# Optimization experiments

Measured on AMD Instinct MI355X. Metric: run time of the kernel, lower is better.

Reference implementation:

```python
import jax, jax.numpy as jnp
import numpy as np

N = 50000      # nodes
E = 800000     # edges
DIN = 500      # input feature dim
H = 128        # hidden dim
C = 40         # num classes
B = 10000      # batch_size (labeled nodes)
L = 9          # n_layers
K = 5          # topk neighbors
ALPHA = 0.5
THETA = 1.0
ETA = 0.5


def setup_inputs() -> dict:
    key = jax.random.key(0)
    ks = jax.random.split(key, 10)
    x = jax.random.normal(ks[0], (N, DIN), jnp.float32)
    edge_index = jax.random.randint(ks[1], (2, E), 0, N, dtype=jnp.int32)
    edge_weight = jax.random.uniform(ks[2], (E,), jnp.float32)
    y = jax.random.randint(ks[3], (B,), 0, C, dtype=jnp.int32)
    W1 = jax.random.normal(ks[4], (DIN, H), jnp.float32) * 0.05
    b1 = jnp.zeros((H,), jnp.float32)
    conv_w1 = jax.random.normal(ks[5], (L, H, H), jnp.float32) * 0.05
    conv_w2 = jax.random.normal(ks[6], (L, H, H), jnp.float32) * 0.05
    W2 = jax.random.normal(ks[7], (H, C), jnp.float32) * 0.05
    b2 = jnp.zeros((C,), jnp.float32)
    return dict(x=x, edge_index=edge_index, edge_weight=edge_weight, y=y,
                batch_size=B, W1=W1, b1=b1, conv_w1=conv_w1, conv_w2=conv_w2,
                W2=W2, b2=b2)


def _spmm(edge_index, edge_weight, h):
    # out[row] += w * h[col]  (sparse adj_t @ h)
    row, col = edge_index[0], edge_index[1]
    msg = h[col] * edge_weight[:, None]           # [E, H]
    return jax.ops.segment_sum(msg, row, num_segments=N)


def reference(x, edge_index, edge_weight, y, batch_size, W1, b1, conv_w1, conv_w2, W2, b2):
    # eval mode: dropout is identity, no diagonal mask in label fusion
    h = jax.nn.relu(x @ W1 + b1)                  # [N, H]
    x0 = h
    for l in range(L):
        beta = float(np.log(THETA / (l + 1) + 1.0))
        p = _spmm(edge_index, edge_weight, h) * (1.0 - ALPHA)   # propagated, scaled
        xr = ALPHA * x0                                          # initial residual
        out = ((1.0 - beta) * p + beta * (p @ conv_w1[l])
               + (1.0 - beta) * xr + beta * (xr @ conv_w2[l]))
        h = jax.nn.relu(h + out)
    emb = h[:batch_size]                          # [B, H]
    logits = h @ W2 + b2
    p_lc = jax.nn.log_softmax(logits[:batch_size], axis=1)       # [B, C]
    # kNN label fusion: cosine similarity, topk, exp-weighted one-hot sum
    an = emb / jnp.clip(jnp.linalg.norm(emb, axis=1, keepdims=True), 1e-8)
    sim = an @ an.T                               # [B, B]
    vals, idx = jax.lax.top_k(sim, K)             # [B, K]
    w = jnp.exp(jax.lax.stop_gradient(vals))      # topk computed under no_grad
    onehot = jax.nn.one_hot(y, C, dtype=jnp.float32)             # [B, C]
    fused = jnp.einsum('bk,bkc->bc', w, onehot[idx])             # [B, C]
    p_sim = jax.nn.log_softmax(fused, axis=1)
    final = ETA * p_lc + (1.0 - ETA) * p_sim
    return final, emb
```

## Files before the change

### kernel.cpp

```cpp
#include <hip/hip_runtime.h>
#include <hip/hip_bf16.h>
#include <math.h>

#define Nn  50000
#define NR  50048
#define En  800000
#define DIN 500
#define Hd  128
#define Cc  40
#define Bb  10000
#define Ll  9
#define KT  5

typedef short bf16x8 __attribute__((ext_vector_type(8)));
typedef unsigned short u16x8 __attribute__((ext_vector_type(8)));
typedef float f32x4 __attribute__((ext_vector_type(4)));

__device__ inline float bf2f(unsigned short u) {
  union { unsigned int i; float f; } c; c.i = (unsigned int)u << 16; return c.f;
}
__device__ inline unsigned short f2bf(float f) {
  __hip_bfloat16 b = __float2bfloat16(f);
  return *(unsigned short*)&b;
}

__global__ __launch_bounds__(256) void k_pack_w1(const float* __restrict__ W1,
                                                 unsigned short* __restrict__ W1p) {
  const int id = blockIdx.x * 256 + threadIdx.x;
  if (id >= 65536) return;
  const int j = id & 7, col = (id >> 3) & 127, qk = id >> 10;
  const int k = (qk >> 2) * 32 + (qk & 3) * 8 + j;
  W1p[id] = f2bf((k < DIN) ? W1[(size_t)k * Hd + col] : 0.f);
}

__global__ __launch_bounds__(256) void k_pack_wc(const float* __restrict__ cw1,
    const float* __restrict__ cw2, unsigned short* __restrict__ Wcp) {
  const int id = blockIdx.x * 256 + threadIdx.x;
  if (id >= 294912) return;
  const int j = id & 7, col = (id >> 3) & 127, qk = (id >> 10) & 31, l = id >> 15;
  const int k = (qk >> 2) * 32 + (qk & 3) * 8 + j;
  float v;
  if (k < 128) v = cw1[((size_t)l * 128 + k) * 128 + col];
  else         v = 0.5f * cw2[((size_t)l * 128 + (k - 128)) * 128 + col];
  Wcp[id] = f2bf(v);
}

__global__ __launch_bounds__(256) void k_in(const float* __restrict__ x,
    const unsigned short* __restrict__ W1p, const float* __restrict__ b1,
    unsigned short* __restrict__ hb, unsigned short* __restrict__ x0b) {
  const int tid = threadIdx.x;
  const int wv = tid >> 6, lane = tid & 63;
  const int lrow = lane & 15, quad = lane >> 4;
  const int row0 = blockIdx.x * 64;
  const int ar = row0 + wv * 16 + lrow;
  f32x4 acc[8];
#pragma unroll
  for (int t = 0; t < 8; ++t) acc[t] = (f32x4){0.f, 0.f, 0.f, 0.f};

  for (int kk = 0; kk < 16; ++kk) {
    const int kbase = kk * 32 + quad * 8;
    float av[8];
    if (ar < Nn) {
      if (kk < 15) {
        const float4 p0 = *(const float4*)(x + (size_t)ar * DIN + kbase);
        const float4 p1 = *(const float4*)(x + (size_t)ar * DIN + kbase + 4);
        av[0] = p0.x; av[1] = p0.y; av[2] = p0.z; av[3] = p0.w;
        av[4] = p1.x; av[5] = p1.y; av[6] = p1.z; av[7] = p1.w;
      } else {
#pragma unroll
        for (int j = 0; j < 8; ++j)
          av[j] = (kbase + j < DIN) ? x[(size_t)ar * DIN + kbase + j] : 0.f;
      }
    } else {
#pragma unroll
      for (int j = 0; j < 8; ++j) av[j] = 0.f;
    }
    bf16x8 af;
#pragma unroll
    for (int j = 0; j < 8; ++j) af[j] = (short)f2bf(av[j]);
#pragma unroll
    for (int nt = 0; nt < 8; ++nt) {
      const bf16x8 bf = *(const bf16x8*)(W1p + ((size_t)(kk * 4 + quad) * 128 + nt * 16 + lrow) * 8);
      acc[nt] = __builtin_amdgcn_mfma_f32_16x16x32_bf16(af, bf, acc[nt], 0, 0, 0);
    }
  }

  __shared__ float sacc[64 * 132];
#pragma unroll
  for (int nt = 0; nt < 8; ++nt)
#pragma unroll
    for (int i = 0; i < 4; ++i)
      sacc[(wv * 16 + quad * 4 + i) * 132 + nt * 16 + lrow] = acc[nt][i];
  __syncthreads();

  const int row = tid >> 2, cs = (tid & 3) * 32;
  const int gr = row0 + row;
  if (gr < Nn) {
#pragma unroll
    for (int g = 0; g < 4; ++g) {
      const int c0 = cs + g * 8;
      float v[8];
#pragma unroll
      for (int j = 0; j < 8; ++j)
        v[j] = fmaxf(sacc[row * 132 + c0 + j] + b1[c0 + j], 0.f);
      u16x8 ob;
#pragma unroll
      for (int j = 0; j < 8; ++j) ob[j] = f2bf(v[j]);
      *(u16x8*)(hb + (size_t)gr * Hd + c0) = ob;
      *(u16x8*)(x0b + (size_t)gr * Hd + c0) = ob;
    }
  }
}

__global__ void k_hist(const int* __restrict__ rows, int* __restrict__ counts) {
  int e = blockIdx.x * 256 + threadIdx.x;
  if (e < En) atomicAdd(&counts[rows[e]], 1);
}

__global__ __launch_bounds__(1024) void k_scan(const int* __restrict__ counts,
                                               int* __restrict__ ptr) {
  __shared__ int buf[1024];
  __shared__ int s_base;
  const int tid = threadIdx.x;
  if (tid == 0) { s_base = 0; ptr[0] = 0; }
  __syncthreads();
  for (int start = 0; start < Nn; start += 1024) {
    int i = start + tid;
    int v = (i < Nn) ? counts[i] : 0;
    buf[tid] = v;
    __syncthreads();
    for (int off = 1; off < 1024; off <<= 1) {
      int t = (tid >= off) ? buf[tid - off] : 0;
      __syncthreads();
      buf[tid] += t;
      __syncthreads();
    }
    if (i < Nn) ptr[i + 1] = s_base + buf[tid];
    __syncthreads();
    if (tid == 0) s_base += buf[1023];
    __syncthreads();
  }
}

__global__ void k_scatter(const int* __restrict__ rows, const int* __restrict__ cols,
                          const float* __restrict__ w, const int* __restrict__ ptr,
                          int* __restrict__ fill, int* __restrict__ csr_col,
                          float* __restrict__ csr_w) {
  int e = blockIdx.x * 256 + threadIdx.x;
  if (e >= En) return;
  int r = rows[e];
  int pos = atomicAdd(&fill[r], 1);
  int d = ptr[r] + pos;
  csr_col[d] = cols[e];
  csr_w[d] = w[e];
}

__global__ __launch_bounds__(256) void k_spmm(const int* __restrict__ ptr,
    const int* __restrict__ csr_col, const float* __restrict__ csr_w,
    const unsigned short* __restrict__ hb, unsigned short* __restrict__ pb) {
  const int wave = (blockIdx.x * 256 + threadIdx.x) >> 6;
  const int lane = threadIdx.x & 63;
  const int g = lane >> 4;
  const int fl = lane & 15;
  if (wave >= Nn) return;
  const int s = ptr[wave], e_end = ptr[wave + 1];
  float acc[8];
#pragma unroll
  for (int j = 0; j < 8; ++j) acc[j] = 0.f;

  auto acc8 = [&](uint4 v, float w) {
    union { unsigned int i; float f; } t;
    t.i = v.x << 16;         acc[0] += w * t.f;
    t.i = v.x & 0xFFFF0000u; acc[1] += w * t.f;
    t.i = v.y << 16;         acc[2] += w * t.f;
    t.i = v.y & 0xFFFF0000u; acc[3] += w * t.f;
    t.i = v.z << 16;         acc[4] += w * t.f;
    t.i = v.z & 0xFFFF0000u; acc[5] += w * t.f;
    t.i = v.w << 16;         acc[6] += w * t.f;
    t.i = v.w & 0xFFFF0000u; acc[7] += w * t.f;
  };

  int e = s + g;
  for (; e + 12 < e_end; e += 16) {
    const int c0 = csr_col[e];
    const int c1 = csr_col[e + 4];
    const int c2 = csr_col[e + 8];
    const int c3 = csr_col[e + 12];
    const float w0 = csr_w[e];
    const float w1 = csr_w[e + 4];
    const float w2 = csr_w[e + 8];
    const float w3 = csr_w[e + 12];
    const uint4 v0 = *(const uint4*)(hb + (size_t)c0 * Hd + fl * 8);
    const uint4 v1 = *(const uint4*)(hb + (size_t)c1 * Hd + fl * 8);
    const uint4 v2 = *(const uint4*)(hb + (size_t)c2 * Hd + fl * 8);
    const uint4 v3 = *(const uint4*)(hb + (size_t)c3 * Hd + fl * 8);
    acc8(v0, w0); acc8(v1, w1); acc8(v2, w2); acc8(v3, w3);
  }
  for (; e + 4 < e_end; e += 8) {
    const int c0 = csr_col[e];
    const int c1 = csr_col[e + 4];
    const float w0 = csr_w[e];
    const float w1 = csr_w[e + 4];
    const uint4 v0 = *(const uint4*)(hb + (size_t)c0 * Hd + fl * 8);
    const uint4 v1 = *(const uint4*)(hb + (size_t)c1 * Hd + fl * 8);
    acc8(v0, w0); acc8(v1, w1);
  }
  if (e < e_end) {
    const int c = csr_col[e];
    const float w = csr_w[e];
    const uint4 v = *(const uint4*)(hb + (size_t)c * Hd + fl * 8);
    acc8(v, w);
  }
#pragma unroll
  for (int j = 0; j < 8; ++j) acc[j] += __shfl_xor(acc[j], 16);
#pragma unroll
  for (int j = 0; j < 8; ++j) acc[j] += __shfl_xor(acc[j], 32);
  if (g == 0) {
    uint4 o;
    o.x = (unsigned int)f2bf(0.5f * acc[0]) | ((unsigned int)f2bf(0.5f * acc[1]) << 16);
    o.y = (unsigned int)f2bf(0.5f * acc[2]) | ((unsigned int)f2bf(0.5f * acc[3]) << 16);
    o.z = (unsigned int)f2bf(0.5f * acc[4]) | ((unsigned int)f2bf(0.5f * acc[5]) << 16);
    o.w = (unsigned int)f2bf(0.5f * acc[6]) | ((unsigned int)f2bf(0.5f * acc[7]) << 16);
    *(uint4*)(pb + (size_t)wave * Hd + fl * 8) = o;
  }
}

__global__ __launch_bounds__(256) void k_layer(const unsigned short* __restrict__ pb,
    const unsigned short* __restrict__ x0b, const unsigned short* __restrict__ Wcp,
    unsigned short* __restrict__ hb, float beta) {
  const int tid = threadIdx.x;
  const int wv = tid >> 6, lane = tid & 63;
  const int lrow = lane & 15, quad = lane >> 4;
  const int row0 = blockIdx.x * 64;
  const int ar = row0 + wv * 16 + lrow;
  f32x4 acc[8];
#pragma unroll
  for (int t = 0; t < 8; ++t) acc[t] = (f32x4){0.f, 0.f, 0.f, 0.f};

#pragma unroll
  for (int kk = 0; kk < 8; ++kk) {
    const unsigned short* src = (kk < 4) ? pb : x0b;
    const int ko = (kk & 3) * 32 + quad * 8;
    const bf16x8 af = *(const bf16x8*)(src + (size_t)ar * Hd + ko);
#pragma unroll
    for (int nt = 0; nt < 8; ++nt) {
      const bf16x8 bf = *(const bf16x8*)(Wcp + ((size_t)(kk * 4 + quad) * 128 + nt * 16 + lrow) * 8);
      acc[nt] = __builtin_amdgcn_mfma_f32_16x16x32_bf16(af, bf, acc[nt], 0, 0, 0);
    }
  }

  __shared__ float sacc[64 * 132];
#pragma unroll
  for (int nt = 0; nt < 8; ++nt)
#pragma unroll
    for (int i = 0; i < 4; ++i)
      sacc[(wv * 16 + quad * 4 + i) * 132 + nt * 16 + lrow] = acc[nt][i];
  __syncthreads();

  const int row = tid >> 2, cs = (tid & 3) * 32;
  const int gr = row0 + row;
  if (gr < Nn) {
    const float om = 1.f - beta;
#pragma unroll
    for (int g = 0; g < 4; ++g) {
      const int c0 = cs + g * 8;
      const u16x8 pv = *(const u16x8*)(pb + (size_t)gr * Hd + c0);
      const u16x8 xv = *(const u16x8*)(x0b + (size_t)gr * Hd + c0);
      const u16x8 hv = *(const u16x8*)(hb + (size_t)gr * Hd + c0);
      float nv[8];
#pragma unroll
      for (int j = 0; j < 8; ++j) {
        const float gemm = sacc[row * 132 + c0 + j];
        const float pj = bf2f(pv[j]);
        const float xj = bf2f(xv[j]);
        const float outv = om * (pj + 0.5f * xj) + beta * gemm;
        nv[j] = fmaxf(bf2f(hv[j]) + outv, 0.f);
      }
      u16x8 ob;
#pragma unroll
      for (int j = 0; j < 8; ++j) ob[j] = f2bf(nv[j]);
      *(u16x8*)(hb + (size_t)gr * Hd + c0) = ob;
    }
  }
}

__global__ __launch_bounds__(256) void k_head(const unsigned short* __restrict__ hb,
    const float* __restrict__ W2, const float* __restrict__ b2,
    unsigned short* __restrict__ anb, float* __restrict__ p_lc,
    float* __restrict__ out_emb) {
  const int wid = (blockIdx.x * 256 + threadIdx.x) >> 6;
  const int lane = threadIdx.x & 63;
  if (wid >= Bb) return;
  const unsigned short* hr = hb + (size_t)wid * Hd;
  const float v0 = bf2f(hr[lane]), v1 = bf2f(hr[lane + 64]);
  out_emb[wid * Hd + lane] = v0;
  out_emb[wid * Hd + lane + 64] = v1;
  float ss = v0 * v0 + v1 * v1;
#pragma unroll
  for (int off = 32; off > 0; off >>= 1) ss += __shfl_xor(ss, off);
  const float inv = 1.f / fmaxf(sqrtf(ss), 1e-8f);
  anb[wid * Hd + lane] = f2bf(v0 * inv);
  anb[wid * Hd + lane + 64] = f2bf(v1 * inv);
  float l = 0.f;
  if (lane < Cc) {
    for (int k = 0; k < Hd; ++k) l += bf2f(hr[k]) * W2[k * Cc + lane];
    l += b2[lane];
  }
  float lm = (lane < Cc) ? l : -3.0e38f;
#pragma unroll
  for (int off = 32; off > 0; off >>= 1) lm = fmaxf(lm, __shfl_xor(lm, off));
  float ex = (lane < Cc) ? expf(l - lm) : 0.f;
#pragma unroll
  for (int off = 32; off > 0; off >>= 1) ex += __shfl_xor(ex, off);
  const float lse = logf(ex);
  if (lane < Cc) p_lc[wid * Cc + lane] = l - lm - lse;
}

#define CH_N  4
#define CH_SZ 2500
#define SB_LD 136
__global__ __launch_bounds__(256) void k_simtopk(const unsigned short* __restrict__ anb,
    float* __restrict__ cval, int* __restrict__ cidx) {
  __shared__ __align__(16) char smem[40960];
  unsigned short* sb = (unsigned short*)smem;
  const int rt = blockIdx.x / CH_N;
  const int chunk = blockIdx.x % CH_N;
  const int row0 = rt * 64;
  const int cbeg = chunk * CH_SZ;
  const int cend = cbeg + CH_SZ;
  const int tid = threadIdx.x;
  const int wv = tid >> 6;
  const int lane = tid & 63;
  const int lrow = lane & 15;
  const int quad = lane >> 4;

  union Frag { uint4 u4; bf16x8 v; };
  bf16x8 afr[4];
  const int ar = row0 + wv * 16 + lrow;
#pragma unroll
  for (int kq = 0; kq < 4; ++kq) {
    Frag f;
    f.u4 = make_uint4(0u, 0u, 0u, 0u);
    if (ar < Bb) f.u4 = *(const uint4*)(anb + (size_t)ar * Hd + kq * 32 + quad * 8);
    afr[kq] = f.v;
  }

  float bv[4][KT];
  int bi[4][KT];
#pragma unroll
  for (int r = 0; r < 4; ++r)
#pragma unroll
    for (int t = 0; t < KT; ++t) { bv[r][t] = -3.0e38f; bi[r][t] = 0x7fffffff; }

  const int ntile = (CH_SZ + 63) / 64;
  for (int t = 0; t < ntile; ++t) {
    const int c0 = cbeg + t * 64;
    __syncthreads();
    for (int i = tid; i < 1024; i += 256) {
      const int r = i >> 4, ch = i & 15;
      const int gc = c0 + r;
      uint4 v = make_uint4(0u, 0u, 0u, 0u);
      if (gc < cend) v = *(const uint4*)(anb + (size_t)gc * Hd + ch * 8);
      *(uint4*)&sb[r * SB_LD + ch * 8] = v;
    }
    __syncthreads();
#pragma unroll
    for (int sub = 0; sub < 4; ++sub) {
      f32x4 acc = {0.f, 0.f, 0.f, 0.f};
      const int scol = sub * 16 + lrow;
#pragma unroll
      for (int kq = 0; kq < 4; ++kq) {
        bf16x8 bfr = *(const bf16x8*)&sb[scol * SB_LD + kq * 32 + quad * 8];
        acc = __builtin_amdgcn_mfma_f32_16x16x32_bf16(afr[kq], bfr, acc, 0, 0, 0);
      }
      const int gc = c0 + scol;
      const bool ok = gc < cend;
#pragma unroll
      for (int i = 0; i < 4; ++i) {
        const float v = ok ? acc[i] : -3.0e38f;
        if (v > bv[i][KT - 1]) {
          float tv = v; int ti = gc;
#pragma unroll
          for (int s = 0; s < KT; ++s) {
            if (tv > bv[i][s]) {
              float ov = bv[i][s]; int oi = bi[i][s];
              bv[i][s] = tv; bi[i][s] = ti; tv = ov; ti = oi;
            }
          }
        }
      }
    }
  }

  __syncthreads();
  float* mv = (float*)smem;
  int* mi = (int*)(smem + 20480);
#pragma unroll
  for (int i = 0; i < 4; ++i) {
    const int row = wv * 16 + quad * 4 + i;
#pragma unroll
    for (int t = 0; t < KT; ++t) {
      mv[row * 80 + lrow * KT + t] = bv[i][t];
      mi[row * 80 + lrow * KT + t] = bi[i][t];
    }
  }
  __syncthreads();
  if (tid < 64) {
    const int gr = row0 + tid;
    if (gr < Bb) {
      float tv5[KT]; int ti5[KT];
#pragma unroll
      for (int t = 0; t < KT; ++t) { tv5[t] = -3.0e38f; ti5[t] = 0x7fffffff; }
      for (int m = 0; m < 80; ++m) {
        float v = mv[tid * 80 + m]; int id = mi[tid * 80 + m];
        if (v > tv5[KT - 1] || (v == tv5[KT - 1] && id < ti5[KT - 1])) {
#pragma unroll
          for (int s = 0; s < KT; ++s) {
            if (v > tv5[s] || (v == tv5[s] && id < ti5[s])) {
              float ov = tv5[s]; int oi = ti5[s];
              tv5[s] = v; ti5[s] = id; v = ov; id = oi;
            }
          }
        }
      }
#pragma unroll
      for (int t = 0; t < KT; ++t) {
        cval[gr * (CH_N * KT) + chunk * KT + t] = tv5[t];
        cidx[gr * (CH_N * KT) + chunk * KT + t] = ti5[t];
      }
    }
  }
}

__global__ __launch_bounds__(256) void k_final(const float* __restrict__ cval,
    const int* __restrict__ cidx, const int* __restrict__ y,
    const float* __restrict__ p_lc, float* __restrict__ out_final) {
  const int b = blockIdx.x * 256 + threadIdx.x;
  if (b >= Bb) return;
  float tv5[KT]; int ti5[KT];
#pragma unroll
  for (int t = 0; t < KT; ++t) { tv5[t] = -3.0e38f; ti5[t] = 0x7fffffff; }
#pragma unroll
  for (int m = 0; m < CH_N * KT; ++m) {
    float v = cval[b * (CH_N * KT) + m]; int id = cidx[b * (CH_N * KT) + m];
    if (v > tv5[KT - 1] || (v == tv5[KT - 1] && id < ti5[KT - 1])) {
#pragma unroll
      for (int t = 0; t < KT; ++t) {
        if (v > tv5[t] || (v == tv5[t] && id < ti5[t])) {
          float ov = tv5[t]; int oi = ti5[t];
          tv5[t] = v; ti5[t] = id; v = ov; id = oi;
        }
      }
    }
  }
  float w[KT]; int cls[KT];
#pragma unroll
  for (int t = 0; t < KT; ++t) { w[t] = expf(tv5[t]); cls[t] = y[ti5[t]]; }
  float m = -3.0e38f;
  for (int c = 0; c < Cc; ++c) {
    float f = 0.f;
#pragma unroll
    for (int t = 0; t < KT; ++t) f += (cls[t] == c) ? w[t] : 0.f;
    m = fmaxf(m, f);
  }
  float s = 0.f;
  for (int c = 0; c < Cc; ++c) {
    float f = 0.f;
#pragma unroll
    for (int t = 0; t < KT; ++t) f += (cls[t] == c) ? w[t] : 0.f;
    s += expf(f - m);
  }
  const float lse = logf(s);
  for (int c = 0; c < Cc; ++c) {
    float f = 0.f;
#pragma unroll
    for (int t = 0; t < KT; ++t) f += (cls[t] == c) ? w[t] : 0.f;
    out_final[b * Cc + c] = 0.5f * p_lc[b * Cc + c] + 0.5f * (f - m - lse);
  }
}

extern "C" void kernel_launch(void* const* d_in, const int* in_sizes, int n_in,
                              void* d_out, int out_size, void* d_ws, size_t ws_size,
                              hipStream_t stream) {
  const float* x  = (const float*)d_in[0];
  const int* erow = (const int*)d_in[1];
  const int* ecol = erow + En;
  const float* ew = (const float*)d_in[2];
  const int* y    = (const int*)d_in[3];
  const float* W1 = (const float*)d_in[5];
  const float* b1 = (const float*)d_in[6];
  const float* cw1 = (const float*)d_in[7];
  const float* cw2 = (const float*)d_in[8];
  const float* W2 = (const float*)d_in[9];
  const float* b2 = (const float*)d_in[10];
  float* out = (float*)d_out;

  float* ws = (float*)d_ws;
  size_t off = 0;
  float* plc = ws + off; off += (size_t)Bb * Cc;
  float* cval = ws + off; off += (size_t)Bb * (CH_N * KT);
  int* cidx  = (int*)(ws + off); off += (size_t)Bb * (CH_N * KT);
  int* counts = (int*)(ws + off); off += Nn;
  int* fill   = (int*)(ws + off); off += Nn;
  int* rptr   = (int*)(ws + off); off += Nn + 4;
  int* ccol   = (int*)(ws + off); off += En;
  float* cwt  = ws + off; off += En;
  unsigned short* anb = (unsigned short*)(ws + off); off += (size_t)Bb * Hd / 2;
  unsigned short* hb  = (unsigned short*)(ws + off); off += (size_t)NR * Hd / 2;
  unsigned short* x0b = (unsigned short*)(ws + off); off += (size_t)NR * Hd / 2;
  unsigned short* pb  = (unsigned short*)(ws + off); off += (size_t)NR * Hd / 2;
  unsigned short* W1p = (unsigned short*)(ws + off); off += 65536 / 2;
  unsigned short* Wcp = (unsigned short*)(ws + off); off += 294912 / 2;

  k_pack_w1<<<256, 256, 0, stream>>>(W1, W1p);
  k_pack_wc<<<1152, 256, 0, stream>>>(cw1, cw2, Wcp);
  k_in<<<NR / 64, 256, 0, stream>>>(x, W1p, b1, hb, x0b);
  hipMemsetAsync(counts, 0, (size_t)2 * Nn * sizeof(int), stream);
  k_hist<<<(En + 255) / 256, 256, 0, stream>>>(erow, counts);
  k_scan<<<1, 1024, 0, stream>>>(counts, rptr);
  k_scatter<<<(En + 255) / 256, 256, 0, stream>>>(erow, ecol, ew, rptr, fill, ccol, cwt);
  for (int l = 0; l < Ll; ++l) {
    const float beta = logf(1.0f / (float)(l + 1) + 1.0f);
    k_spmm<<<(Nn * 64 + 255) / 256, 256, 0, stream>>>(rptr, ccol, cwt, hb, pb);
    k_layer<<<NR / 64, 256, 0, stream>>>(pb, x0b, Wcp + (size_t)l * 32768, hb, beta);
  }
  k_head<<<(Bb * 64) / 256, 256, 0, stream>>>(hb, W2, b2, anb, plc, out + (size_t)Bb * Cc);
  k_simtopk<<<((Bb + 63) / 64) * CH_N, 256, 0, stream>>>(anb, cval, cidx);
  k_final<<<(Bb + 255) / 256, 256, 0, stream>>>(cval, cidx, y, plc, out);
}
```

Before: 1.066 ms.

## Bucket CSR edges by column range and run SpMM in four cache-local passes

Sorts each row's edges into four column buckets during CSR construction and splits the sparse aggregation into four passes, each gathering only from one quarter of the feature matrix. The intent is to make gathers of h hit a cache-resident slice. In exchange, partial sums go through an fp32 accumulator buffer with read-modify-write each pass, and launch count and row-pointer reads grow fourfold.

```diff
diff --git a/kernel.cpp b/kernel.cpp
--- a/kernel.cpp
+++ b/kernel.cpp
@@ -11,6 +11,8 @@
 #define Bb  10000
 #define Ll  9
 #define KT  5
+#define NB  4
+#define BSZ 12500
 
 typedef short bf16x8 __attribute__((ext_vector_type(8)));
 typedef unsigned short u16x8 __attribute__((ext_vector_type(8)));
@@ -112,12 +114,15 @@
   }
 }
 
-__global__ void k_hist(const int* __restrict__ rows, int* __restrict__ counts) {
+__global__ void k_hist(const int* __restrict__ rows, const int* __restrict__ cols,
+                       int* __restrict__ counts_rb) {
   int e = blockIdx.x * 256 + threadIdx.x;
-  if (e < En) atomicAdd(&counts[rows[e]], 1);
-}
-
-__global__ __launch_bounds__(1024) void k_scan(const int* __restrict__ counts,
+  if (e >= En) return;
+  int b = cols[e] / BSZ;  if (b > NB - 1) b = NB - 1;
+  atomicAdd(&counts_rb[rows[e] * NB + b], 1);
+}
+
+__global__ __launch_bounds__(1024) void k_scan(const int* __restrict__ counts_rb,
                                                int* __restrict__ ptr) {
   __shared__ int buf[1024];
   __shared__ int s_base;
@@ -126,7 +131,11 @@
   __syncthreads();
   for (int start = 0; start < Nn; start += 1024) {
     int i = start + tid;
-    int v = (i < Nn) ? counts[i] : 0;
+    int v = 0;
+    if (i < Nn) {
+      const int4 c = *(const int4*)(counts_rb + i * NB);
+      v = c.x + c.y + c.z + c.w;
+    }
     buf[tid] = v;
     __syncthreads();
     for (int off = 1; off < 1024; off <<= 1) {
@@ -142,28 +151,46 @@
   }
 }
 
+__global__ __launch_bounds__(256) void k_bucketptr(const int* __restrict__ counts_rb,
+    const int* __restrict__ rptr, int* __restrict__ ptr2) {
+  const int row = blockIdx.x * 256 + threadIdx.x;
+  if (row >= Nn) return;
+  const int4 c = *(const int4*)(counts_rb + row * NB);
+  const int base = rptr[row];
+  int4 o;
+  o.x = base;
+  o.y = base + c.x;
+  o.z = base + c.x + c.y;
+  o.w = base + c.x + c.y + c.z;
+  *(int4*)(ptr2 + row * NB) = o;
+  if (row == 0) ptr2[NB * Nn] = En;
+}
+
 __global__ void k_scatter(const int* __restrict__ rows, const int* __restrict__ cols,
-                          const float* __restrict__ w, const int* __restrict__ ptr,
-                          int* __restrict__ fill, int* __restrict__ csr_col,
+                          const float* __restrict__ w, const int* __restrict__ ptr2,
+                          int* __restrict__ fill2, int* __restrict__ csr_col,
                           float* __restrict__ csr_w) {
   int e = blockIdx.x * 256 + threadIdx.x;
   if (e >= En) return;
   int r = rows[e];
-  int pos = atomicAdd(&fill[r], 1);
-  int d = ptr[r] + pos;
-  csr_col[d] = cols[e];
+  int c = cols[e];
+  int b = c / BSZ;  if (b > NB - 1) b = NB - 1;
+  int pos = atomicAdd(&fill2[r * NB + b], 1);
+  int d = ptr2[r * NB + b] + pos;
+  csr_col[d] = c;
   csr_w[d] = w[e];
 }
 
-__global__ __launch_bounds__(256) void k_spmm(const int* __restrict__ ptr,
+__global__ __launch_bounds__(256) void k_spmm_pass(const int* __restrict__ ptr2,
     const int* __restrict__ csr_col, const float* __restrict__ csr_w,
-    const unsigned short* __restrict__ hb, unsigned short* __restrict__ pb) {
+    const unsigned short* __restrict__ hb, float* __restrict__ pacc,
+    unsigned short* __restrict__ pb, int bkt) {
   const int wave = (blockIdx.x * 256 + threadIdx.x) >> 6;
   const int lane = threadIdx.x & 63;
   const int g = lane >> 4;
   const int fl = lane & 15;
   if (wave >= Nn) return;
-  const int s = ptr[wave], e_end = ptr[wave + 1];
+  const int s = ptr2[wave * NB + bkt], e_end = ptr2[wave * NB + bkt + 1];
   float acc[8];
 #pragma unroll
   for (int j = 0; j < 8; ++j) acc[j] = 0.f;
@@ -216,12 +243,29 @@
 #pragma unroll
   for (int j = 0; j < 8; ++j) acc[j] += __shfl_xor(acc[j], 32);
   if (g == 0) {
-    uint4 o;
-    o.x = (unsigned int)f2bf(0.5f * acc[0]) | ((unsigned int)f2bf(0.5f * acc[1]) << 16);
-    o.y = (unsigned int)f2bf(0.5f * acc[2]) | ((unsigned int)f2bf(0.5f * acc[3]) << 16);
-    o.z = (unsigned int)f2bf(0.5f * acc[4]) | ((unsigned int)f2bf(0.5f * acc[5]) << 16);
-    o.w = (unsigned int)f2bf(0.5f * acc[6]) | ((unsigned int)f2bf(0.5f * acc[7]) << 16);
-    *(uint4*)(pb + (size_t)wave * Hd + fl * 8) = o;
+    float* pr = pacc + (size_t)wave * Hd + fl * 8;
+    if (bkt == 0) {
+      float4 a = {acc[0], acc[1], acc[2], acc[3]};
+      float4 b = {acc[4], acc[5], acc[6], acc[7]};
+      *(float4*)pr = a;
+      *(float4*)(pr + 4) = b;
+    } else if (bkt < NB - 1) {
+      float4 a = *(const float4*)pr;
+      float4 b = *(const float4*)(pr + 4);
+      a.x += acc[0]; a.y += acc[1]; a.z += acc[2]; a.w += acc[3];
+      b.x += acc[4]; b.y += acc[5]; b.z += acc[6]; b.w += acc[7];
+      *(float4*)pr = a;
+      *(float4*)(pr + 4) = b;
+    } else {
+      const float4 a = *(const float4*)pr;
+      const float4 b = *(const float4*)(pr + 4);
+      uint4 o;
+      o.x = (unsigned int)f2bf(0.5f * (a.x + acc[0])) | ((unsigned int)f2bf(0.5f * (a.y + acc[1])) << 16);
+      o.y = (unsigned int)f2bf(0.5f * (a.z + acc[2])) | ((unsigned int)f2bf(0.5f * (a.w + acc[3])) << 16);
+      o.z = (unsigned int)f2bf(0.5f * (b.x + acc[4])) | ((unsigned int)f2bf(0.5f * (b.y + acc[5])) << 16);
+      o.w = (unsigned int)f2bf(0.5f * (b.z + acc[6])) | ((unsigned int)f2bf(0.5f * (b.w + acc[7])) << 16);
+      *(uint4*)(pb + (size_t)wave * Hd + fl * 8) = o;
+    }
   }
 }
 
@@ -500,11 +544,13 @@
   float* plc = ws + off; off += (size_t)Bb * Cc;
   float* cval = ws + off; off += (size_t)Bb * (CH_N * KT);
   int* cidx  = (int*)(ws + off); off += (size_t)Bb * (CH_N * KT);
-  int* counts = (int*)(ws + off); off += Nn;
-  int* fill   = (int*)(ws + off); off += Nn;
-  int* rptr   = (int*)(ws + off); off += Nn + 4;
-  int* ccol   = (int*)(ws + off); off += En;
-  float* cwt  = ws + off; off += En;
+  int* counts_rb = (int*)(ws + off); off += (size_t)Nn * NB;
+  int* fill2     = (int*)(ws + off); off += (size_t)Nn * NB;
+  int* rptr  = (int*)(ws + off); off += Nn + 4;
+  int* ptr2  = (int*)(ws + off); off += (size_t)Nn * NB + 4;
+  int* ccol  = (int*)(ws + off); off += En;
+  float* cwt = ws + off; off += En;
+  float* pacc = ws + off; off += (size_t)NR * Hd;
   unsigned short* anb = (unsigned short*)(ws + off); off += (size_t)Bb * Hd / 2;
   unsigned short* hb  = (unsigned short*)(ws + off); off += (size_t)NR * Hd / 2;
   unsigned short* x0b = (unsigned short*)(ws + off); off += (size_t)NR * Hd / 2;
@@ -515,13 +561,15 @@
   k_pack_w1<<<256, 256, 0, stream>>>(W1, W1p);
   k_pack_wc<<<1152, 256, 0, stream>>>(cw1, cw2, Wcp);
   k_in<<<NR / 64, 256, 0, stream>>>(x, W1p, b1, hb, x0b);
-  hipMemsetAsync(counts, 0, (size_t)2 * Nn * sizeof(int), stream);
-  k_hist<<<(En + 255) / 256, 256, 0, stream>>>(erow, counts);
-  k_scan<<<1, 1024, 0, stream>>>(counts, rptr);
-  k_scatter<<<(En + 255) / 256, 256, 0, stream>>>(erow, ecol, ew, rptr, fill, ccol, cwt);
+  hipMemsetAsync(counts_rb, 0, (size_t)2 * Nn * NB * sizeof(int), stream);
+  k_hist<<<(En + 255) / 256, 256, 0, stream>>>(erow, ecol, counts_rb);
+  k_scan<<<1, 1024, 0, stream>>>(counts_rb, rptr);
+  k_bucketptr<<<(Nn + 255) / 256, 256, 0, stream>>>(counts_rb, rptr, ptr2);
+  k_scatter<<<(En + 255) / 256, 256, 0, stream>>>(erow, ecol, ew, ptr2, fill2, ccol, cwt);
   for (int l = 0; l < Ll; ++l) {
     const float beta = logf(1.0f / (float)(l + 1) + 1.0f);
-    k_spmm<<<(Nn * 64 + 255) / 256, 256, 0, stream>>>(rptr, ccol, cwt, hb, pb);
+    for (int b = 0; b < NB; ++b)
+      k_spmm_pass<<<(Nn * 64 + 255) / 256, 256, 0, stream>>>(ptr2, ccol, cwt, hb, pacc, pb, b);
     k_layer<<<NR / 64, 256, 0, stream>>>(pb, x0b, Wcp + (size_t)l * 32768, hb, beta);
   }
   k_head<<<(Bb * 64) / 256, 256, 0, stream>>>(hb, W2, b2, anb, plc, out + (size_t)Bb * Cc);
```

New measurement: 1.463 ms. 1.37x slower.

## Bucket CSR columns by source-node range to improve SpMM gather locality

Applied to the files above, without the earlier changes.

Builds the CSR with each row's edges grouped into 16 column-range buckets. A per-row, per-bucket histogram, a bucket pointer kernel and a bucketed scatter replace the plain per-row fill. The aim is to make the nine SpMM passes gather h rows in a more locality-friendly order across waves, improving L2 hit rates. It adds a 16x larger histogram and fill array, an extra kernel, a bigger memset and more atomic traffic during CSR construction.

```diff
diff --git a/kernel.cpp b/kernel.cpp
--- a/kernel.cpp
+++ b/kernel.cpp
@@ -11,6 +11,8 @@
 #define Bb  10000
 #define Ll  9
 #define KT  5
+#define NB  16
+#define BSZ 3125
 
 typedef short bf16x8 __attribute__((ext_vector_type(8)));
 typedef unsigned short u16x8 __attribute__((ext_vector_type(8)));
@@ -112,12 +114,15 @@
   }
 }
 
-__global__ void k_hist(const int* __restrict__ rows, int* __restrict__ counts) {
+__global__ void k_hist(const int* __restrict__ rows, const int* __restrict__ cols,
+                       int* __restrict__ counts_rb) {
   int e = blockIdx.x * 256 + threadIdx.x;
-  if (e < En) atomicAdd(&counts[rows[e]], 1);
-}
-
-__global__ __launch_bounds__(1024) void k_scan(const int* __restrict__ counts,
+  if (e >= En) return;
+  int b = cols[e] / BSZ;  if (b > NB - 1) b = NB - 1;
+  atomicAdd(&counts_rb[rows[e] * NB + b], 1);
+}
+
+__global__ __launch_bounds__(1024) void k_scan(const int* __restrict__ counts_rb,
                                                int* __restrict__ ptr) {
   __shared__ int buf[1024];
   __shared__ int s_base;
@@ -126,7 +131,14 @@
   __syncthreads();
   for (int start = 0; start < Nn; start += 1024) {
     int i = start + tid;
-    int v = (i < Nn) ? counts[i] : 0;
+    int v = 0;
+    if (i < Nn) {
+#pragma unroll
+      for (int b4 = 0; b4 < NB / 4; ++b4) {
+        const int4 c = *(const int4*)(counts_rb + (size_t)i * NB + b4 * 4);
+        v += c.x + c.y + c.z + c.w;
+      }
+    }
     buf[tid] = v;
     __syncthreads();
     for (int off = 1; off < 1024; off <<= 1) {
@@ -142,16 +154,30 @@
   }
 }
 
+__global__ __launch_bounds__(256) void k_bucketptr(const int* __restrict__ counts_rb,
+    const int* __restrict__ rptr, int* __restrict__ ptr2) {
+  const int row = blockIdx.x * 256 + threadIdx.x;
+  if (row >= Nn) return;
+  int base = rptr[row];
+#pragma unroll
+  for (int b = 0; b < NB; ++b) {
+    ptr2[(size_t)row * NB + b] = base;
+    base += counts_rb[(size_t)row * NB + b];
+  }
+}
+
 __global__ void k_scatter(const int* __restrict__ rows, const int* __restrict__ cols,
-                          const float* __restrict__ w, const int* __restrict__ ptr,
-                          int* __restrict__ fill, int* __restrict__ csr_col,
+                          const float* __restrict__ w, const int* __restrict__ ptr2,
+                          int* __restrict__ fill2, int* __restrict__ csr_col,
                           float* __restrict__ csr_w) {
   int e = blockIdx.x * 256 + threadIdx.x;
   if (e >= En) return;
   int r = rows[e];
-  int pos = atomicAdd(&fill[r], 1);
-  int d = ptr[r] + pos;
-  csr_col[d] = cols[e];
+  int c = cols[e];
+  int b = c / BSZ;  if (b > NB - 1) b = NB - 1;
+  int pos = atomicAdd(&fill2[(size_t)r * NB + b], 1);
+  int d = ptr2[(size_t)r * NB + b] + pos;
+  csr_col[d] = c;
   csr_w[d] = w[e];
 }
 
@@ -500,11 +526,12 @@
   float* plc = ws + off; off += (size_t)Bb * Cc;
   float* cval = ws + off; off += (size_t)Bb * (CH_N * KT);
   int* cidx  = (int*)(ws + off); off += (size_t)Bb * (CH_N * KT);
-  int* counts = (int*)(ws + off); off += Nn;
-  int* fill   = (int*)(ws + off); off += Nn;
-  int* rptr   = (int*)(ws + off); off += Nn + 4;
-  int* ccol   = (int*)(ws + off); off += En;
-  float* cwt  = ws + off; off += En;
+  int* counts_rb = (int*)(ws + off); off += (size_t)Nn * NB;
+  int* fill2     = (int*)(ws + off); off += (size_t)Nn * NB;
+  int* rptr  = (int*)(ws + off); off += Nn + 4;
+  int* ptr2  = (int*)(ws + off); off += (size_t)Nn * NB + 4;
+  int* ccol  = (int*)(ws + off); off += En;
+  float* cwt = ws + off; off += En;
   unsigned short* anb = (unsigned short*)(ws + off); off += (size_t)Bb * Hd / 2;
   unsigned short* hb  = (unsigned short*)(ws + off); off += (size_t)NR * Hd / 2;
   unsigned short* x0b = (unsigned short*)(ws + off); off += (size_t)NR * Hd / 2;
@@ -515,10 +542,11 @@
   k_pack_w1<<<256, 256, 0, stream>>>(W1, W1p);
   k_pack_wc<<<1152, 256, 0, stream>>>(cw1, cw2, Wcp);
   k_in<<<NR / 64, 256, 0, stream>>>(x, W1p, b1, hb, x0b);
-  hipMemsetAsync(counts, 0, (size_t)2 * Nn * sizeof(int), stream);
-  k_hist<<<(En + 255) / 256, 256, 0, stream>>>(erow, counts);
-  k_scan<<<1, 1024, 0, stream>>>(counts, rptr);
-  k_scatter<<<(En + 255) / 256, 256, 0, stream>>>(erow, ecol, ew, rptr, fill, ccol, cwt);
+  hipMemsetAsync(counts_rb, 0, (size_t)2 * Nn * NB * sizeof(int), stream);
+  k_hist<<<(En + 255) / 256, 256, 0, stream>>>(erow, ecol, counts_rb);
+  k_scan<<<1, 1024, 0, stream>>>(counts_rb, rptr);
+  k_bucketptr<<<(Nn + 255) / 256, 256, 0, stream>>>(counts_rb, rptr, ptr2);
+  k_scatter<<<(En + 255) / 256, 256, 0, stream>>>(erow, ecol, ew, ptr2, fill2, ccol, cwt);
   for (int l = 0; l < Ll; ++l) {
     const float beta = logf(1.0f / (float)(l + 1) + 1.0f);
     k_spmm<<<(Nn * 64 + 255) / 256, 256, 0, stream>>>(rptr, ccol, cwt, hb, pb);
```

New measurement: 1.111 ms. 4.2% more time.
